# Optimization experiments

Hardware: AMD Instinct MI355X
Metric: run time of the kernel (lower is better)

The kernel has to match this reference:

```python
import jax, jax.numpy as jnp
import numpy as np

B, C, L, D, P = 64, 64, 720, 512, 336
P2, H = P // 2, 512  # H = hidden width of the ProbG branch


def setup_inputs() -> dict:
    key = jax.random.key(0)
    ks = jax.random.split(key, 20)
    def w(k, i, o):
        return jax.random.normal(k, (i, o), jnp.float32) / np.sqrt(i)
    return {
        "x_bsd": jax.random.normal(ks[0], (B, L, C), jnp.float32),
        "z0": jax.random.normal(ks[1], (B, C, D), jnp.float32),
        "y0": jax.random.normal(ks[2], (B, C, P), jnp.float32),
        # ProbG hidden branch (HID_GIVEN_X_V0 -> SS_Z_GIVEN_X_V0)
        "W_h": w(ks[3], L, H),
        "W_ssz": w(ks[4], H, 2 * D),
        # x->z scale/shift flows (versions v2..v5)
        "W_xz_v2": w(ks[5], L, 2 * D),
        "W_xz_v3": w(ks[6], L, 2 * D),
        "W_xz_v4": w(ks[7], L, 2 * D),
        "W_xz_v5": w(ks[8], L, 2 * D),
        # z->x scale/shift flows (v0, v2, v3, v5)
        "W_zx_v0": w(ks[9], D, 2 * L),
        "W_zx_v2": w(ks[10], D, 2 * L),
        "W_zx_v3": w(ks[11], D, 2 * L),
        "W_zx_v5": w(ks[12], D, 2 * L),
        # z->y scale/shift flow (v4, used inside encoding)
        "W_zy_v4": w(ks[13], D, 2 * P),
        # decode heads: ROT_IN_Y_V1 and KOO_Y_GIVEN_Z_V0
        "W_rot": w(ks[14], D, P2),
        "W_koo": w(ks[15], D, 2 * P),
        # Koopman complex params for y-space (a + i b per channel/pair)
        "a_y": jnp.ones((C, P2), jnp.float32),
        "b_y": jnp.zeros((C, P2), jnp.float32) + 0.1,
    }


def _ss(params):
    """Split conditioner output into (positive scale, shift)."""
    s_raw, t = jnp.split(params, 2, axis=-1)
    return jnp.exp(jnp.tanh(s_raw)), t


def _affine(v, cond, W):
    """Scale/shift flow: v <- v * s(cond) + t(cond)."""
    s, t = _ss(jnp.einsum('bck,km->bcm', cond, W))
    return v * s + t


def _rot(u, theta, inv=False):
    """Rotate interleaved (re, im) pairs of u [B,C,P] by angles theta [B,C,P/2]."""
    re, im = u[..., 0::2], u[..., 1::2]
    th = -theta if inv else theta
    c, s = jnp.cos(th), jnp.sin(th)
    return jnp.stack([c * re - s * im, s * re + c * im], axis=-1).reshape(u.shape)


def _koop(u, a, b, inv=False):
    """Koopman unit-complex multiply on interleaved pairs; a,b [C,P/2]."""
    n = jnp.sqrt(a * a + b * b)
    ca, cb = a / n, b / n
    cb = -cb if inv else cb
    re, im = u[..., 0::2], u[..., 1::2]
    return jnp.stack([ca * re - cb * im, cb * re + ca * im], axis=-1).reshape(u.shape)


def reference(x_bsd, z0, y0, W_h, W_ssz, W_xz_v2, W_xz_v3, W_xz_v4, W_xz_v5,
              W_zx_v0, W_zx_v2, W_zx_v3, W_zx_v5, W_zy_v4, W_rot, W_koo, a_y, b_y):
    x = jnp.transpose(x_bsd, (0, 2, 1))  # [B,C,L]
    z = z0 * 0.1                          # [B,C,D]
    y = y0 * 0.1                          # [B,C,P]
    # ---- encoding phase ----
    h = jax.nn.gelu(jnp.einsum('bcl,lk->bck', x, W_h))  # X_to_Z_PROB hidden
    z = _affine(z, h, W_ssz)
    x = _affine(x, z, W_zx_v0)
    z = _affine(z, x, W_xz_v2); x = _affine(x, z, W_zx_v2)
    z = _affine(z, x, W_xz_v3); x = _affine(x, z, W_zx_v3)
    z = _affine(z, x, W_xz_v4); y = _affine(y, z, W_zy_v4)  # Z_to_Y_V4
    z = _affine(z, x, W_xz_v5); x = _affine(x, z, W_zx_v5)
    pre_y = y
    # ---- decode: rotate -> ky -> scale -> ky.inv -> rot.inv -> shift ----
    theta = jnp.pi * jnp.tanh(jnp.einsum('bcd,dp->bcp', z, W_rot))   # [B,C,P/2]
    scale, shift = _ss(jnp.einsum('bcd,dp->bcp', z, W_koo))          # [B,C,P]
    const = _koop(_rot(pre_y, theta), a_y, b_y)
    accu = const * scale
    accu = _rot(_koop(accu, a_y, b_y, inv=True), theta, inv=True) + shift
    return jnp.transpose(accu, (0, 2, 1))  # [B,P,C]
```

## Files before the change

kernel.cpp:

```cpp
#include <hip/hip_runtime.h>
#include <hip/hip_bf16.h>
#include <math.h>

#define BB  64
#define CC  64
#define LL  720
#define LLP 736
#define DD  512
#define PP  336
#define P2C 168
#define HH  512
#define MM  (BB*CC)

typedef _Float16 f16x8 __attribute__((ext_vector_type(8)));
typedef float    f32x4 __attribute__((ext_vector_type(4)));

#define GLDS16(g, l) __builtin_amdgcn_global_load_lds( \
    (const __attribute__((address_space(1))) void*)(g), \
    (__attribute__((address_space(3))) void*)(l), 16, 0, 0)

struct WDesc { const float* src; _Float16* dstHi; _Float16* dstLo;
               int K, N, Kpad, tbase, tilesN; };
struct WTab  { WDesc d[12]; };

__global__ __launch_bounds__(256) void k_convert(WTab tab) {
  __shared__ float tile[16][17];
  const int bid = blockIdx.x;
  int wi = 0;
#pragma unroll
  for (int i = 1; i < 12; ++i) if (bid >= tab.d[i].tbase) wi = i;
  const WDesc d = tab.d[wi];
  const int lt = bid - d.tbase;
  const int tk = lt / d.tilesN, tn = lt % d.tilesN;
  const int k0 = tk * 16, n0 = tn * 16;
  const int tx = threadIdx.x & 15, ty = threadIdx.x >> 4;
  float v = 0.f;
  if (n0 + tx < d.N) v = d.src[(size_t)(k0 + ty) * d.N + n0 + tx];
  tile[ty][tx] = v;
  __syncthreads();
  if (n0 + ty < d.N) {
    const float w = tile[tx][ty];
    const _Float16 h = (_Float16)w;
    const _Float16 l = (_Float16)(w - (float)h);
    const size_t base = (size_t)(n0 + ty) * d.Kpad;
    d.dstHi[base + k0 + tx] = h;
    d.dstLo[base + k0 + tx] = l;
    if (d.Kpad != d.K && k0 + 16 == d.K) {
      d.dstHi[base + d.K + tx] = (_Float16)0.f;
      d.dstLo[base + d.K + tx] = (_Float16)0.f;
    }
  }
}

__global__ __launch_bounds__(256) void k_xpose(const float* __restrict__ xbsd,
                                               _Float16* __restrict__ xhi,
                                               _Float16* __restrict__ xlo) {
  __shared__ float tile[16][17];
  const int b = blockIdx.z, l0 = blockIdx.x * 16, c0 = blockIdx.y * 16;
  const int tx = threadIdx.x, ty = threadIdx.y;
  tile[ty][tx] = xbsd[(size_t)b * LL * CC + (size_t)(l0 + ty) * CC + c0 + tx];
  __syncthreads();
  const float v = tile[tx][ty];
  const _Float16 h = (_Float16)v;
  const _Float16 l = (_Float16)(v - (float)h);
  const size_t m = (size_t)b * CC + c0 + ty;
  xhi[m * LLP + l0 + tx] = h;
  xlo[m * LLP + l0 + tx] = l;
  if (l0 == 704) {
    xhi[m * LLP + 720 + tx] = (_Float16)0.f;
    xlo[m * LLP + 720 + tx] = (_Float16)0.f;
  }
}

template<int EPI, bool DUAL, bool VIN16, bool OUT_T>
__global__ __launch_bounds__(256)
void k_gemm(const _Float16* Ahi, const _Float16* Alo, int lda,
            const _Float16* Whi, const _Float16* Wlo, int ldw,
            const float* Vin32, const _Float16* VinHi,
            const _Float16* VinLo, int ldv, float vscale,
            float* outT32,
            _Float16* outHi, _Float16* outLo, int ldo,
            int Kp, int Nv) {
  constexpr int NB   = DUAL ? 128 : 64;
  constexpr int ABUF = 128 * 32;
  constexpr int BBUF = NB * 32;
  constexpr int BUFH = 2 * ABUF + 2 * BBUF;
  constexpr int NCH  = 16 + 2 * (NB / 16);
  constexpr int NCHW = NCH / 4;
  __shared__ _Float16 smem[2 * BUFH];

  const int m0 = blockIdx.y * 128;
  const int n0 = blockIdx.x * 64;
  const int tid = threadIdx.x;
  const int w = tid >> 6, lane = tid & 63, q = lane >> 4, r = lane & 15;
  const int wr = (w & 1) * 64, wc = (w >> 1) * 32;
  const int lr = lane >> 2, ls = lane & 3;

  f32x4 accS[4][2] = {};
  f32x4 accT[4][2] = {};

  auto issue_dma = [&](int buf, int k0) {
    _Float16* base = &smem[buf * BUFH];
#pragma unroll
    for (int cc = 0; cc < NCHW; ++cc) {
      const int chunk = w * NCHW + cc;
      const _Float16* gsrc;
      _Float16* ldst;
      if (chunk < 8) {
        const int rb = chunk * 16;
        const int R = rb + lr;
        const int ss = ls ^ ((R >> 1) & 3);
        gsrc = Ahi + (size_t)(m0 + R) * lda + k0 + ss * 8;
        ldst = base + rb * 32;
      } else if (chunk < 16) {
        const int rb = (chunk - 8) * 16;
        const int R = rb + lr;
        const int ss = ls ^ ((R >> 1) & 3);
        gsrc = Alo + (size_t)(m0 + R) * lda + k0 + ss * 8;
        ldst = base + ABUF + rb * 32;
      } else if (chunk < 16 + NB / 16) {
        const int rb = (chunk - 16) * 16;
        const int R = rb + lr;
        const int ss = ls ^ ((R >> 1) & 3);
        const int wrow = (R < 64) ? (n0 + R) : (Nv + n0 + (R - 64));
        gsrc = Whi + (size_t)wrow * ldw + k0 + ss * 8;
        ldst = base + 2 * ABUF + rb * 32;
      } else {
        const int rb = (chunk - 16 - NB / 16) * 16;
        const int R = rb + lr;
        const int ss = ls ^ ((R >> 1) & 3);
        const int wrow = (R < 64) ? (n0 + R) : (Nv + n0 + (R - 64));
        gsrc = Wlo + (size_t)wrow * ldw + k0 + ss * 8;
        ldst = base + 2 * ABUF + BBUF + rb * 32;
      }
      GLDS16(gsrc, ldst);
    }
  };

  issue_dma(0, 0);
  const int nk = Kp >> 5;
  for (int kc = 0; kc < nk; ++kc) {
    __syncthreads();
    if (kc + 1 < nk) issue_dma((kc + 1) & 1, (kc + 1) << 5);

    const _Float16* base = &smem[(kc & 1) * BUFH];
    f16x8 ah[4], al[4];
#pragma unroll
    for (int rt = 0; rt < 4; ++rt) {
      const int R = wr + rt * 16 + r;
      const int t = (q ^ ((R >> 1) & 3)) * 8;
      ah[rt] = *(const f16x8*)(base + R * 32 + t);
      al[rt] = *(const f16x8*)(base + ABUF + R * 32 + t);
    }
#pragma unroll
    for (int ct = 0; ct < 2; ++ct) {
      const int RB = wc + ct * 16 + r;
      const int tb = (q ^ ((RB >> 1) & 3)) * 8;
      const f16x8 bh = *(const f16x8*)(base + 2 * ABUF + RB * 32 + tb);
      const f16x8 bl = *(const f16x8*)(base + 2 * ABUF + BBUF + RB * 32 + tb);
#pragma unroll
      for (int rt = 0; rt < 4; ++rt) {
        accS[rt][ct] = __builtin_amdgcn_mfma_f32_16x16x32_f16(ah[rt], bh, accS[rt][ct], 0, 0, 0);
        accS[rt][ct] = __builtin_amdgcn_mfma_f32_16x16x32_f16(al[rt], bh, accS[rt][ct], 0, 0, 0);
        accS[rt][ct] = __builtin_amdgcn_mfma_f32_16x16x32_f16(ah[rt], bl, accS[rt][ct], 0, 0, 0);
      }
      if (DUAL) {
        const int RT = 64 + RB;
        const int tt = (q ^ ((RT >> 1) & 3)) * 8;
        const f16x8 chh = *(const f16x8*)(base + 2 * ABUF + RT * 32 + tt);
        const f16x8 cll = *(const f16x8*)(base + 2 * ABUF + BBUF + RT * 32 + tt);
#pragma unroll
        for (int rt = 0; rt < 4; ++rt) {
          accT[rt][ct] = __builtin_amdgcn_mfma_f32_16x16x32_f16(ah[rt], chh, accT[rt][ct], 0, 0, 0);
          accT[rt][ct] = __builtin_amdgcn_mfma_f32_16x16x32_f16(al[rt], chh, accT[rt][ct], 0, 0, 0);
          accT[rt][ct] = __builtin_amdgcn_mfma_f32_16x16x32_f16(ah[rt], cll, accT[rt][ct], 0, 0, 0);
        }
      }
    }
  }

#pragma unroll
  for (int rt = 0; rt < 4; ++rt) {
    const int mb = m0 + wr + rt * 16 + q * 4;
#pragma unroll
    for (int ct = 0; ct < 2; ++ct) {
      const int n = n0 + wc + ct * 16 + r;
      if (n >= Nv) continue;
      if (EPI == 2) {
        *(f32x4*)(outT32 + (size_t)n * MM + mb) = accS[rt][ct];
      } else if (EPI == 1) {
#pragma unroll
        for (int g = 0; g < 4; ++g) {
          const int m = mb + g;
          const float v = accS[rt][ct][g];
          const float o = 0.5f * v * (1.0f + tanhf(0.7978845608028654f * (v + 0.044715f * v * v * v)));
          const _Float16 h = (_Float16)o;
          outHi[(size_t)m * ldo + n] = h;
          outLo[(size_t)m * ldo + n] = (_Float16)(o - (float)h);
        }
      } else {
        f32x4 o;
#pragma unroll
        for (int g = 0; g < 4; ++g) {
          const int m = mb + g;
          float v;
          if (VIN16) {
            v = (float)VinHi[(size_t)m * ldv + n] + (float)VinLo[(size_t)m * ldv + n];
          } else {
            v = Vin32[(size_t)m * ldv + n];
          }
          const float s = expf(tanhf(accS[rt][ct][g]));
          o[g] = v * vscale * s + accT[rt][ct][g];
        }
        if (OUT_T) {
          *(f32x4*)(outT32 + (size_t)n * MM + mb) = o;
        } else {
#pragma unroll
          for (int g = 0; g < 4; ++g) {
            const int m = mb + g;
            const _Float16 h = (_Float16)o[g];
            outHi[(size_t)m * ldo + n] = h;
            outLo[(size_t)m * ldo + n] = (_Float16)(o[g] - (float)h);
          }
        }
      }
    }
  }
}

__global__ __launch_bounds__(256) void k_final(const float* __restrict__ Pt,
                                               const float* __restrict__ yT,
                                               const float* __restrict__ Ay,
                                               const float* __restrict__ By,
                                               float* __restrict__ out) {
  const int c = threadIdx.x;
  const int j = blockIdx.x * 4 + threadIdx.y;
  const int b = blockIdx.y;
  const int m = b * 64 + c;
  const float th = 3.14159265358979323846f * tanhf(Pt[(size_t)j * MM + m]);
  const float sc0 = expf(tanhf(Pt[(size_t)(168 + 2 * j) * MM + m]));
  const float sc1 = expf(tanhf(Pt[(size_t)(169 + 2 * j) * MM + m]));
  const float t0 = Pt[(size_t)(504 + 2 * j) * MM + m];
  const float t1 = Pt[(size_t)(505 + 2 * j) * MM + m];
  const float re = yT[(size_t)(2 * j) * MM + m];
  const float im = yT[(size_t)(2 * j + 1) * MM + m];
  const float a = Ay[c * P2C + j], bb = By[c * P2C + j];
  const float rn = rsqrtf(a * a + bb * bb);
  const float ca = a * rn, cb = bb * rn;
  float s1v, c1;
  sincosf(th, &s1v, &c1);
  const float r1 = c1 * re - s1v * im, i1 = s1v * re + c1 * im;
  const float r2 = ca * r1 - cb * i1,  i2 = cb * r1 + ca * i1;
  const float r3 = r2 * sc0,           i3 = i2 * sc1;
  const float r4 = ca * r3 + cb * i3,  i4 = ca * i3 - cb * r3;
  const float r5 = c1 * r4 + s1v * i4, i5 = c1 * i4 - s1v * r4;
  out[(size_t)b * PP * CC + (size_t)(2 * j) * CC + c]     = r5 + t0;
  out[(size_t)b * PP * CC + (size_t)(2 * j + 1) * CC + c] = i5 + t1;
}

extern "C" void kernel_launch(void* const* d_in, const int* in_sizes, int n_in,
                              void* d_out, int out_size, void* d_ws, size_t ws_size,
                              hipStream_t stream) {
  const float* x_bsd   = (const float*)d_in[0];
  const float* z0      = (const float*)d_in[1];
  const float* y0      = (const float*)d_in[2];
  const float* W_h     = (const float*)d_in[3];
  const float* W_ssz   = (const float*)d_in[4];
  const float* W_xz_v2 = (const float*)d_in[5];
  const float* W_xz_v3 = (const float*)d_in[6];
  const float* W_xz_v4 = (const float*)d_in[7];
  const float* W_xz_v5 = (const float*)d_in[8];
  const float* W_zx_v0 = (const float*)d_in[9];
  const float* W_zx_v2 = (const float*)d_in[10];
  const float* W_zx_v3 = (const float*)d_in[11];
  const float* W_zy_v4 = (const float*)d_in[13];
  const float* W_rot   = (const float*)d_in[14];
  const float* W_koo   = (const float*)d_in[15];
  const float* a_y     = (const float*)d_in[16];
  const float* b_y     = (const float*)d_in[17];
  float* out = (float*)d_out;

  char* p = (char*)d_ws;
  auto alloc = [&](size_t bytes) -> void* {
    void* r = (void*)p; p += (bytes + 255) & ~(size_t)255; return r;
  };
  float*    yT  = (float*)alloc((size_t)PP * MM * 4);
  float*    Pt  = (float*)alloc((size_t)(P2C * 5) * MM * 4);
  _Float16* xhi = (_Float16*)alloc((size_t)MM * LLP * 2);
  _Float16* xlo = (_Float16*)alloc((size_t)MM * LLP * 2);
  _Float16* zhi = (_Float16*)alloc((size_t)MM * DD * 2);
  _Float16* zlo = (_Float16*)alloc((size_t)MM * DD * 2);
  _Float16* hhi = (_Float16*)alloc((size_t)MM * HH * 2);
  _Float16* hlo = (_Float16*)alloc((size_t)MM * HH * 2);
  auto wpair = [&](size_t elems, _Float16** lo) -> _Float16* {
    _Float16* hi = (_Float16*)alloc(elems * 2);
    *lo = (_Float16*)alloc(elems * 2);
    return hi;
  };
  _Float16 *tWhL, *tWsszL, *tWxz2L, *tWxz3L, *tWxz4L, *tWxz5L;
  _Float16 *tWzx0L, *tWzx2L, *tWzx3L, *tWzyL, *tWcatL;
  _Float16* tWh   = wpair((size_t)HH * LLP, &tWhL);
  _Float16* tWssz = wpair((size_t)(2*DD) * DD, &tWsszL);
  _Float16* tWxz2 = wpair((size_t)(2*DD) * LLP, &tWxz2L);
  _Float16* tWxz3 = wpair((size_t)(2*DD) * LLP, &tWxz3L);
  _Float16* tWxz4 = wpair((size_t)(2*DD) * LLP, &tWxz4L);
  _Float16* tWxz5 = wpair((size_t)(2*DD) * LLP, &tWxz5L);
  _Float16* tWzx0 = wpair((size_t)1536 * DD, &tWzx0L);
  _Float16* tWzx2 = wpair((size_t)1536 * DD, &tWzx2L);
  _Float16* tWzx3 = wpair((size_t)1536 * DD, &tWzx3L);
  _Float16* tWzy  = wpair((size_t)768 * DD, &tWzyL);
  _Float16* tWcat = wpair((size_t)896 * DD, &tWcatL);

  WTab tab;
  int base = 0;
  auto put = [&](int i, const float* src, _Float16* dh, _Float16* dl,
                 int K, int N, int Kpad) {
    const int tN = (N + 15) / 16;
    tab.d[i] = WDesc{src, dh, dl, K, N, Kpad, base, tN};
    base += ((K + 15) / 16) * tN;
  };
  put(0,  W_h,     tWh,   tWhL,   LL, HH,   LLP);
  put(1,  W_ssz,   tWssz, tWsszL, DD, 2*DD, DD);
  put(2,  W_xz_v2, tWxz2, tWxz2L, LL, 2*DD, LLP);
  put(3,  W_xz_v3, tWxz3, tWxz3L, LL, 2*DD, LLP);
  put(4,  W_xz_v4, tWxz4, tWxz4L, LL, 2*DD, LLP);
  put(5,  W_xz_v5, tWxz5, tWxz5L, LL, 2*DD, LLP);
  put(6,  W_zx_v0, tWzx0, tWzx0L, DD, 2*LL, DD);
  put(7,  W_zx_v2, tWzx2, tWzx2L, DD, 2*LL, DD);
  put(8,  W_zx_v3, tWzx3, tWzx3L, DD, 2*LL, DD);
  put(9,  W_zy_v4, tWzy,  tWzyL,  DD, 2*PP, DD);
  put(10, W_rot,   tWcat, tWcatL, DD, P2C,  DD);
  put(11, W_koo,   tWcat + (size_t)P2C * DD, tWcatL + (size_t)P2C * DD, DD, 2*PP, DD);
  const int total_tiles = base;

  k_convert<<<dim3(total_tiles), dim3(256), 0, stream>>>(tab);
  k_xpose<<<dim3(45, 4, 64), dim3(16, 16), 0, stream>>>(x_bsd, xhi, xlo);

  const dim3 blk(256);
  k_gemm<1, false, false, false><<<dim3(8, 32), blk, 0, stream>>>(
      xhi, xlo, LLP, tWh, tWhL, LLP,
      nullptr, nullptr, nullptr, 0, 0.f, nullptr, hhi, hlo, HH, LLP, HH);
  k_gemm<0, true, false, false><<<dim3(8, 32), blk, 0, stream>>>(
      hhi, hlo, HH, tWssz, tWsszL, DD,
      z0, nullptr, nullptr, DD, 0.1f, nullptr, zhi, zlo, DD, DD, DD);
  k_gemm<0, true, true, false><<<dim3(12, 32), blk, 0, stream>>>(
      zhi, zlo, DD, tWzx0, tWzx0L, DD,
      nullptr, xhi, xlo, LLP, 1.f, nullptr, xhi, xlo, LLP, DD, LL);
  k_gemm<0, true, true, false><<<dim3(8, 32), blk, 0, stream>>>(
      xhi, xlo, LLP, tWxz2, tWxz2L, LLP,
      nullptr, zhi, zlo, DD, 1.f, nullptr, zhi, zlo, DD, LLP, DD);
  k_gemm<0, true, true, false><<<dim3(12, 32), blk, 0, stream>>>(
      zhi, zlo, DD, tWzx2, tWzx2L, DD,
      nullptr, xhi, xlo, LLP, 1.f, nullptr, xhi, xlo, LLP, DD, LL);
  k_gemm<0, true, true, false><<<dim3(8, 32), blk, 0, stream>>>(
      xhi, xlo, LLP, tWxz3, tWxz3L, LLP,
      nullptr, zhi, zlo, DD, 1.f, nullptr, zhi, zlo, DD, LLP, DD);
  k_gemm<0, true, true, false><<<dim3(12, 32), blk, 0, stream>>>(
      zhi, zlo, DD, tWzx3, tWzx3L, DD,
      nullptr, xhi, xlo, LLP, 1.f, nullptr, xhi, xlo, LLP, DD, LL);
  k_gemm<0, true, true, false><<<dim3(8, 32), blk, 0, stream>>>(
      xhi, xlo, LLP, tWxz4, tWxz4L, LLP,
      nullptr, zhi, zlo, DD, 1.f, nullptr, zhi, zlo, DD, LLP, DD);
  k_gemm<0, true, false, true><<<dim3(6, 32), blk, 0, stream>>>(
      zhi, zlo, DD, tWzy, tWzyL, DD,
      y0, nullptr, nullptr, PP, 0.1f, yT, nullptr, nullptr, 0, DD, PP);
  k_gemm<0, true, true, false><<<dim3(8, 32), blk, 0, stream>>>(
      xhi, xlo, LLP, tWxz5, tWxz5L, LLP,
      nullptr, zhi, zlo, DD, 1.f, nullptr, zhi, zlo, DD, LLP, DD);
  k_gemm<2, false, false, true><<<dim3(14, 32), blk, 0, stream>>>(
      zhi, zlo, DD, tWcat, tWcatL, DD,
      nullptr, nullptr, nullptr, 0, 0.f, Pt, nullptr, nullptr, 0, DD, P2C * 5);
  k_final<<<dim3(42, 64), dim3(64, 4), 0, stream>>>(Pt, yT, a_y, b_y, out);
}
```

Measured before the change: 491.7 us.

## Shrink GEMM M-tile to 64 rows and drop double-buffered LDS prefetch

Halves the GEMM block tile along M from 128 to 64 rows and doubles the grid in y, so each launch has twice as many workgroups. It also removes the double-buffered async global-to-LDS prefetch and uses a single buffer with a barrier before and after compute. The aim is more parallelism across CUs and lower LDS use per block, at the cost of less weight reuse per tile and no overlap between loads and MFMA.

```diff
diff --git a/kernel.cpp b/kernel.cpp
--- a/kernel.cpp
+++ b/kernel.cpp
@@ -82,84 +82,77 @@
             _Float16* outHi, _Float16* outLo, int ldo,
             int Kp, int Nv) {
   constexpr int NB   = DUAL ? 128 : 64;
-  constexpr int ABUF = 128 * 32;
+  constexpr int ABUF = 64 * 32;
   constexpr int BBUF = NB * 32;
-  constexpr int BUFH = 2 * ABUF + 2 * BBUF;
-  constexpr int NCH  = 16 + 2 * (NB / 16);
+  constexpr int NCH  = 8 + 2 * (NB / 16);
   constexpr int NCHW = NCH / 4;
-  __shared__ _Float16 smem[2 * BUFH];
-
-  const int m0 = blockIdx.y * 128;
+  __shared__ _Float16 smem[2 * ABUF + 2 * BBUF];
+
+  const int m0 = blockIdx.y * 64;
   const int n0 = blockIdx.x * 64;
   const int tid = threadIdx.x;
   const int w = tid >> 6, lane = tid & 63, q = lane >> 4, r = lane & 15;
-  const int wr = (w & 1) * 64, wc = (w >> 1) * 32;
+  const int wr = (w & 1) * 32, wc = (w >> 1) * 32;
   const int lr = lane >> 2, ls = lane & 3;
 
-  f32x4 accS[4][2] = {};
-  f32x4 accT[4][2] = {};
-
-  auto issue_dma = [&](int buf, int k0) {
-    _Float16* base = &smem[buf * BUFH];
+  f32x4 accS[2][2] = {};
+  f32x4 accT[2][2] = {};
+
+  const int nk = Kp >> 5;
+  for (int kc = 0; kc < nk; ++kc) {
+    const int k0 = kc << 5;
 #pragma unroll
     for (int cc = 0; cc < NCHW; ++cc) {
       const int chunk = w * NCHW + cc;
       const _Float16* gsrc;
       _Float16* ldst;
-      if (chunk < 8) {
+      if (chunk < 4) {
         const int rb = chunk * 16;
         const int R = rb + lr;
         const int ss = ls ^ ((R >> 1) & 3);
         gsrc = Ahi + (size_t)(m0 + R) * lda + k0 + ss * 8;
-        ldst = base + rb * 32;
-      } else if (chunk < 16) {
-        const int rb = (chunk - 8) * 16;
+        ldst = smem + rb * 32;
+      } else if (chunk < 8) {
+        const int rb = (chunk - 4) * 16;
         const int R = rb + lr;
         const int ss = ls ^ ((R >> 1) & 3);
         gsrc = Alo + (size_t)(m0 + R) * lda + k0 + ss * 8;
-        ldst = base + ABUF + rb * 32;
-      } else if (chunk < 16 + NB / 16) {
-        const int rb = (chunk - 16) * 16;
+        ldst = smem + ABUF + rb * 32;
+      } else if (chunk < 8 + NB / 16) {
+        const int rb = (chunk - 8) * 16;
         const int R = rb + lr;
         const int ss = ls ^ ((R >> 1) & 3);
         const int wrow = (R < 64) ? (n0 + R) : (Nv + n0 + (R - 64));
         gsrc = Whi + (size_t)wrow * ldw + k0 + ss * 8;
-        ldst = base + 2 * ABUF + rb * 32;
+        ldst = smem + 2 * ABUF + rb * 32;
       } else {
-        const int rb = (chunk - 16 - NB / 16) * 16;
+        const int rb = (chunk - 8 - NB / 16) * 16;
         const int R = rb + lr;
         const int ss = ls ^ ((R >> 1) & 3);
         const int wrow = (R < 64) ? (n0 + R) : (Nv + n0 + (R - 64));
         gsrc = Wlo + (size_t)wrow * ldw + k0 + ss * 8;
-        ldst = base + 2 * ABUF + BBUF + rb * 32;
+        ldst = smem + 2 * ABUF + BBUF + rb * 32;
       }
       GLDS16(gsrc, ldst);
     }
-  };
-
-  issue_dma(0, 0);
-  const int nk = Kp >> 5;
-  for (int kc = 0; kc < nk; ++kc) {
     __syncthreads();
-    if (kc + 1 < nk) issue_dma((kc + 1) & 1, (kc + 1) << 5);
-
-    const _Float16* base = &smem[(kc & 1) * BUFH];
-    f16x8 ah[4], al[4];
-#pragma unroll
-    for (int rt = 0; rt < 4; ++rt) {
+
+    f16x8 ah[2], al[2];
+#pragma unroll
+    for (int rt = 0; rt < 2; ++rt) {
       const int R = wr + rt * 16 + r;
       const int t = (q ^ ((R >> 1) & 3)) * 8;
-      ah[rt] = *(const f16x8*)(base + R * 32 + t);
-      al[rt] = *(const f16x8*)(base + ABUF + R * 32 + t);
+      ah[rt] = *(const f16x8*)(smem + R * 32 + t);
+      al[rt] = *(const f16x8*)(smem + ABUF + R * 32 + t);
     }
 #pragma unroll
     for (int ct = 0; ct < 2; ++ct) {
       const int RB = wc + ct * 16 + r;
       const int tb = (q ^ ((RB >> 1) & 3)) * 8;
-      const f16x8 bh = *(const f16x8*)(base + 2 * ABUF + RB * 32 + tb);
-      const f16x8 bl = *(const f16x8*)(base + 2 * ABUF + BBUF + RB * 32 + tb);
-#pragma unroll
-      for (int rt = 0; rt < 4; ++rt) {
+      const f16x8 bh = *(const f16x8*)(smem + 2 * ABUF + RB * 32 + tb);
+      const f16x8 bl = *(const f16x8*)(smem + 2 * ABUF + BBUF + RB * 32 + tb);
+#pragma unroll
+      for (int rt = 0; rt < 2; ++rt) {
         accS[rt][ct] = __builtin_amdgcn_mfma_f32_16x16x32_f16(ah[rt], bh, accS[rt][ct], 0, 0, 0);
         accS[rt][ct] = __builtin_amdgcn_mfma_f32_16x16x32_f16(al[rt], bh, accS[rt][ct], 0, 0, 0);
         accS[rt][ct] = __builtin_amdgcn_mfma_f32_16x16x32_f16(ah[rt], bl, accS[rt][ct], 0, 0, 0);
@@ -167,20 +160,21 @@
       if (DUAL) {
         const int RT = 64 + RB;
         const int tt = (q ^ ((RT >> 1) & 3)) * 8;
-        const f16x8 chh = *(const f16x8*)(base + 2 * ABUF + RT * 32 + tt);
-        const f16x8 cll = *(const f16x8*)(base + 2 * ABUF + BBUF + RT * 32 + tt);
-#pragma unroll
-        for (int rt = 0; rt < 4; ++rt) {
+        const f16x8 chh = *(const f16x8*)(smem + 2 * ABUF + RT * 32 + tt);
+        const f16x8 cll = *(const f16x8*)(smem + 2 * ABUF + BBUF + RT * 32 + tt);
+#pragma unroll
+        for (int rt = 0; rt < 2; ++rt) {
           accT[rt][ct] = __builtin_amdgcn_mfma_f32_16x16x32_f16(ah[rt], chh, accT[rt][ct], 0, 0, 0);
           accT[rt][ct] = __builtin_amdgcn_mfma_f32_16x16x32_f16(al[rt], chh, accT[rt][ct], 0, 0, 0);
           accT[rt][ct] = __builtin_amdgcn_mfma_f32_16x16x32_f16(ah[rt], cll, accT[rt][ct], 0, 0, 0);
         }
       }
     }
+    __syncthreads();
   }
 
 #pragma unroll
-  for (int rt = 0; rt < 4; ++rt) {
+  for (int rt = 0; rt < 2; ++rt) {
     const int mb = m0 + wr + rt * 16 + q * 4;
 #pragma unroll
     for (int ct = 0; ct < 2; ++ct) {
@@ -337,37 +331,37 @@
   k_xpose<<<dim3(45, 4, 64), dim3(16, 16), 0, stream>>>(x_bsd, xhi, xlo);
 
   const dim3 blk(256);
-  k_gemm<1, false, false, false><<<dim3(8, 32), blk, 0, stream>>>(
+  k_gemm<1, false, false, false><<<dim3(8, 64), blk, 0, stream>>>(
       xhi, xlo, LLP, tWh, tWhL, LLP,
       nullptr, nullptr, nullptr, 0, 0.f, nullptr, hhi, hlo, HH, LLP, HH);
-  k_gemm<0, true, false, false><<<dim3(8, 32), blk, 0, stream>>>(
+  k_gemm<0, true, false, false><<<dim3(8, 64), blk, 0, stream>>>(
       hhi, hlo, HH, tWssz, tWsszL, DD,
       z0, nullptr, nullptr, DD, 0.1f, nullptr, zhi, zlo, DD, DD, DD);
-  k_gemm<0, true, true, false><<<dim3(12, 32), blk, 0, stream>>>(
+  k_gemm<0, true, true, false><<<dim3(12, 64), blk, 0, stream>>>(
       zhi, zlo, DD, tWzx0, tWzx0L, DD,
       nullptr, xhi, xlo, LLP, 1.f, nullptr, xhi, xlo, LLP, DD, LL);
-  k_gemm<0, true, true, false><<<dim3(8, 32), blk, 0, stream>>>(
+  k_gemm<0, true, true, false><<<dim3(8, 64), blk, 0, stream>>>(
       xhi, xlo, LLP, tWxz2, tWxz2L, LLP,
       nullptr, zhi, zlo, DD, 1.f, nullptr, zhi, zlo, DD, LLP, DD);
-  k_gemm<0, true, true, false><<<dim3(12, 32), blk, 0, stream>>>(
+  k_gemm<0, true, true, false><<<dim3(12, 64), blk, 0, stream>>>(
       zhi, zlo, DD, tWzx2, tWzx2L, DD,
       nullptr, xhi, xlo, LLP, 1.f, nullptr, xhi, xlo, LLP, DD, LL);
-  k_gemm<0, true, true, false><<<dim3(8, 32), blk, 0, stream>>>(
+  k_gemm<0, true, true, false><<<dim3(8, 64), blk, 0, stream>>>(
       xhi, xlo, LLP, tWxz3, tWxz3L, LLP,
       nullptr, zhi, zlo, DD, 1.f, nullptr, zhi, zlo, DD, LLP, DD);
-  k_gemm<0, true, true, false><<<dim3(12, 32), blk, 0, stream>>>(
+  k_gemm<0, true, true, false><<<dim3(12, 64), blk, 0, stream>>>(
       zhi, zlo, DD, tWzx3, tWzx3L, DD,
       nullptr, xhi, xlo, LLP, 1.f, nullptr, xhi, xlo, LLP, DD, LL);
-  k_gemm<0, true, true, false><<<dim3(8, 32), blk, 0, stream>>>(
+  k_gemm<0, true, true, false><<<dim3(8, 64), blk, 0, stream>>>(
       xhi, xlo, LLP, tWxz4, tWxz4L, LLP,
       nullptr, zhi, zlo, DD, 1.f, nullptr, zhi, zlo, DD, LLP, DD);
-  k_gemm<0, true, false, true><<<dim3(6, 32), blk, 0, stream>>>(
+  k_gemm<0, true, false, true><<<dim3(6, 64), blk, 0, stream>>>(
       zhi, zlo, DD, tWzy, tWzyL, DD,
       y0, nullptr, nullptr, PP, 0.1f, yT, nullptr, nullptr, 0, DD, PP);
-  k_gemm<0, true, true, false><<<dim3(8, 32), blk, 0, stream>>>(
+  k_gemm<0, true, true, false><<<dim3(8, 64), blk, 0, stream>>>(
       xhi, xlo, LLP, tWxz5, tWxz5L, LLP,
       nullptr, zhi, zlo, DD, 1.f, nullptr, zhi, zlo, DD, LLP, DD);
-  k_gemm<2, false, false, true><<<dim3(14, 32), blk, 0, stream>>>(
+  k_gemm<2, false, false, true><<<dim3(14, 64), blk, 0, stream>>>(
       zhi, zlo, DD, tWcat, tWcatL, DD,
       nullptr, nullptr, nullptr, 0, 0.f, Pt, nullptr, nullptr, 0, DD, P2C * 5);
   k_final<<<dim3(42, 64), dim3(64, 4), 0, stream>>>(Pt, yT, a_y, b_y, out);
```

New measurement: 476.4 us. 3.1% less time.
